# Kernel tuning notes

Hardware: AMD Instinct MI355X
Metric: run time of the kernel (lower is better)

Reference implementation:

```python
import jax, jax.numpy as jnp
import numpy as np

D_MODEL = 2048
N_HEADS = 16
D_HEAD = 128
ROPE_THETA = 10000.0


def _rope(x, offset):
    # x: [B, H, S, D]; half-rotation RoPE with position offset
    B, H, S, D = x.shape
    inv_freq = 1.0 / (ROPE_THETA ** (jnp.arange(0, D, 2, dtype=jnp.float32) / D))  # [D/2]
    pos = (offset + jnp.arange(S, dtype=jnp.float32))                              # [S]
    ang = pos[:, None] * inv_freq[None, :]                                         # [S, D/2]
    cos = jnp.cos(ang).astype(x.dtype)
    sin = jnp.sin(ang).astype(x.dtype)
    x1, x2 = x[..., : D // 2], x[..., D // 2 :]
    return jnp.concatenate([x1 * cos - x2 * sin, x2 * cos + x1 * sin], axis=-1)


def setup_inputs() -> dict:
    key = jax.random.key(0)
    ks = jax.random.split(key, 5)
    B, Sq, Skv = 4, 1024, 1024
    x = jax.random.normal(ks[0], (B, Sq, D_MODEL), dtype=jnp.float32)
    cache_k = jax.random.normal(ks[1], (B, N_HEADS, Skv, D_HEAD), dtype=jnp.float32)
    cache_v = jax.random.normal(ks[2], (B, N_HEADS, Skv, D_HEAD), dtype=jnp.float32)
    w_qkv = jax.random.normal(ks[3], (D_MODEL, 3 * D_MODEL), dtype=jnp.float32) * (D_MODEL ** -0.5)
    w_o = jax.random.normal(ks[4], (D_MODEL, D_MODEL), dtype=jnp.float32) * (D_MODEL ** -0.5)
    return {"x": x, "cache_k": cache_k, "cache_v": cache_v, "w_qkv": w_qkv, "w_o": w_o}


def reference(x, cache_k, cache_v, w_qkv, w_o):
    B, S, _ = x.shape
    offset = cache_k.shape[2]
    # fused QKV projection: [B, S, 3*d_model] -> [B, H, S, 3*d_head]
    qkv = jnp.einsum("bsd,de->bse", x, w_qkv)
    qkv = qkv.reshape(B, S, N_HEADS, 3 * D_HEAD).transpose(0, 2, 1, 3)
    q, k, v = jnp.split(qkv, 3, axis=-1)
    q = _rope(q, offset)
    k = _rope(k, offset)
    # KV-cache concat along sequence dim
    k = jnp.concatenate([cache_k, k], axis=2)  # [B, H, Skv+S, D]
    v = jnp.concatenate([cache_v, v], axis=2)
    # SDPA (no mask, matching mask=None path)
    scale = D_HEAD ** -0.5
    scores = jnp.einsum("bhqd,bhkd->bhqk", q, k) * scale
    attn = jax.nn.softmax(scores, axis=-1)
    out = jnp.einsum("bhqk,bhkd->bhqd", attn, v)           # [B, H, S, D]
    out = out.transpose(0, 2, 1, 3).reshape(B, S, D_MODEL)
    return jnp.einsum("bsd,de->bse", out, w_o)
```

## Files before the change

### kernel.cpp

```cpp
#include <hip/hip_runtime.h>


typedef __bf16 bf16x8 __attribute__((ext_vector_type(8)));
typedef float f32x4 __attribute__((ext_vector_type(4)));
typedef unsigned short u16x8 __attribute__((ext_vector_type(8)));
typedef unsigned short u16x4 __attribute__((ext_vector_type(4)));

__device__ __forceinline__ float b2f(unsigned short u) {
  return __builtin_bit_cast(float, (unsigned int)u << 16);
}
__device__ __forceinline__ unsigned short f2b(float f) {
  unsigned int x = __builtin_bit_cast(unsigned int, f);
  x += 0x7fffu + ((x >> 16) & 1u);
  return (unsigned short)(x >> 16);
}
__device__ __forceinline__ unsigned int cvt_pk_bf16(float lo, float hi) {
  unsigned int r;
  asm("v_cvt_pk_bf16_f32 %0, %1, %2" : "=v"(r) : "v"(lo), "v"(hi));
  return r;
}
__device__ __forceinline__ void gload_lds16(const void* g, void* l) {
  __builtin_amdgcn_global_load_lds(
      (__attribute__((address_space(1))) void*)(g),
      (__attribute__((address_space(3))) void*)(l), 16, 0, 0);
}
__device__ __forceinline__ void barrier_nodrain() {
  asm volatile("" ::: "memory");
  __builtin_amdgcn_s_barrier();
  asm volatile("" ::: "memory");
}

__global__ __launch_bounds__(256) void prep_fused(
    const float* __restrict__ x, const float* __restrict__ ck,
    const float* __restrict__ cv, const float* __restrict__ wqkv,
    const float* __restrict__ wo, unsigned short* __restrict__ xb,
    unsigned short* __restrict__ Kf, unsigned short* __restrict__ Vt,
    unsigned short* __restrict__ wqT, unsigned short* __restrict__ woT,
    float* __restrict__ cs, float* __restrict__ sn) {
  __shared__ float tile[32][33];
  int id = blockIdx.x;
  if (id < 4096) {
    size_t i = ((size_t)id * 256 + threadIdx.x) * 8;
    float4 a = *(const float4*)(x + i);
    float4 b = *(const float4*)(x + i + 4);
    u16x8 v;
    v[0] = f2b(a.x); v[1] = f2b(a.y); v[2] = f2b(a.z); v[3] = f2b(a.w);
    v[4] = f2b(b.x); v[5] = f2b(b.y); v[6] = f2b(b.z); v[7] = f2b(b.w);
    *(u16x8*)(xb + i) = v;
  } else if (id < 20480) {
    const float* in;  unsigned short* out;  int R, C, idx;
    if (id < 16384) { in = wqkv; out = wqT; R = 2048; C = 6144; idx = id - 4096; }
    else            { in = wo;   out = woT; R = 2048; C = 2048; idx = id - 16384; }
    int nc = C >> 5;
    int c0 = (idx % nc) * 32, r0 = (idx / nc) * 32;
    int tx = threadIdx.x & 31, ty = threadIdx.x >> 5;
#pragma unroll
    for (int j = 0; j < 4; ++j)
      tile[ty + j * 8][tx] = in[(size_t)(r0 + ty + j * 8) * C + c0 + tx];
    __syncthreads();
#pragma unroll
    for (int j = 0; j < 4; ++j)
      out[(size_t)(c0 + ty + j * 8) * R + r0 + tx] = f2b(tile[tx][ty + j * 8]);
  } else if (id < 28672) {
    size_t idx = ((size_t)(id - 20480) * 256 + threadIdx.x) * 4;
    size_t bh = idx >> 17, rem = idx & 131071;
    float4 a = *(const float4*)(ck + idx);
    u16x4 v;
    v[0] = f2b(a.x); v[1] = f2b(a.y); v[2] = f2b(a.z); v[3] = f2b(a.w);
    *(u16x4*)(Kf + bh * 262144 + rem) = v;
  } else if (id < 28928) {
    int idx = (id - 28672) * 256 + threadIdx.x;
    int s = idx >> 6, i = idx & 63;
    float inv = exp2f(-(float)i * (13.287712379549449f / 64.0f));
    float ang = (float)(1024 + s) * inv;
    cs[idx] = cosf(ang);
    sn[idx] = sinf(ang);
  } else {
    int idx = id - 28928;
    int bhid = idx >> 7;
    int rem = idx & 127;
    int d0 = (rem >> 5) * 32, s0 = (rem & 31) * 32;
    int tx = threadIdx.x & 31, ty = threadIdx.x >> 5;
#pragma unroll
    for (int j = 0; j < 4; ++j)
      tile[ty + j * 8][tx] = cv[((size_t)bhid * 1024 + s0 + ty + j * 8) * 128 + d0 + tx];
    __syncthreads();
#pragma unroll
    for (int j = 0; j < 4; ++j)
      Vt[((size_t)bhid * 128 + d0 + ty + j * 8) * 2048 + s0 + tx] =
          f2b(tile[tx][ty + j * 8]);
  }
}

template <int M, int N, int K, int MODE>
__global__ __launch_bounds__(512, 4) void gemm_ring(
    const unsigned short* __restrict__ A, const unsigned short* __restrict__ B,
    void* __restrict__ Cout, const float* __restrict__ cs,
    const float* __restrict__ sn, unsigned short* __restrict__ Qb,
    unsigned short* __restrict__ Kf, unsigned short* __restrict__ Vt) {
  __shared__ __align__(16) char lds[3 * 24576];
  constexpr int NT = N / 128;
  constexpr int Kt = K / 32;
  int bid = blockIdx.x;
  int tm = bid / NT, tn = bid % NT;
  int tid = threadIdx.x;
  int lane = tid & 63, wave = tid >> 6;
  int wr = (wave >> 1) * 64;
  int wc1 = wave & 1;
  int l15 = lane & 15, g = lane >> 4;
  int rcol = (g * 16) ^ (((l15 >> 1) & 3) << 4);

  int p = tid * 16;
  int srcCol = (p & 63) ^ (((p >> 7) & 3) << 4);
  const unsigned short* aSrc0 = A + (size_t)(tm * 256 + (p >> 6)) * K + (srcCol >> 1);
  const unsigned short* aSrc1 = aSrc0 + (size_t)128 * K;
  const unsigned short* bSrc  = B + (size_t)(tn * 128 + (p >> 6)) * K + (srcCol >> 1);

  f32x4 acc[4][4] = {};

  auto stage = [&](int s) {
    char* base = (char*)lds + s * 24576;
    gload_lds16(aSrc0, base + p);
    gload_lds16(aSrc1, base + 8192 + p);
    gload_lds16(bSrc,  base + 16384 + p);
    aSrc0 += 32; aSrc1 += 32; bSrc += 32;
  };

  stage(0);
  stage(1);
  asm volatile("s_waitcnt vmcnt(3)" ::: "memory");

  int slot = 0, sNext = 2;
  for (int t = 0; t < Kt; ++t) {
    barrier_nodrain();
    if (t + 2 < Kt) {
      stage(sNext);
      sNext = (sNext == 2) ? 0 : sNext + 1;
      asm volatile("s_waitcnt vmcnt(3)" ::: "memory");
    } else {
      asm volatile("s_waitcnt vmcnt(0)" ::: "memory");
    }
    const char* As_ = (const char*)lds + slot * 24576;
    const char* Bs_ = As_ + 16384;
    bf16x8 af[4], bfr[4];
#pragma unroll
    for (int m = 0; m < 4; ++m)
      af[m] = *(const bf16x8*)(As_ + (wr + m * 16 + l15) * 64 + rcol);
#pragma unroll
    for (int n = 0; n < 4; ++n)
      bfr[n] = *(const bf16x8*)(Bs_ + (wc1 * 16 + n * 32 + l15) * 64 + rcol);
    __builtin_amdgcn_s_setprio(1);
#pragma unroll
    for (int m = 0; m < 4; ++m)
#pragma unroll
      for (int n = 0; n < 4; ++n)
        acc[m][n] = __builtin_amdgcn_mfma_f32_16x16x32_bf16(af[m], bfr[n], acc[m][n], 0, 0, 0);
    __builtin_amdgcn_s_setprio(0);
    slot = (slot == 2) ? 0 : slot + 1;
  }

  if constexpr (MODE == 0) {
#pragma unroll
    for (int m = 0; m < 4; ++m) {
      int row0 = tm * 256 + wr + m * 16 + g * 4;
#pragma unroll
      for (int n = 0; n < 4; ++n) {
        int col = tn * 128 + wc1 * 16 + n * 32 + l15;
#pragma unroll
        for (int r = 0; r < 4; ++r)
          ((float*)Cout)[(size_t)(row0 + r) * N + col] = acc[m][n][r];
      }
    }
  } else {
    int part = tn % 3, h = tn / 3;
    size_t bh = (size_t)(tm >> 2) * 16 + h;
    if (part == 2) {
#pragma unroll
      for (int m = 0; m < 4; ++m) {
        int s0 = (tm & 3) * 256 + wr + m * 16 + g * 4;
#pragma unroll
        for (int n = 0; n < 4; ++n) {
          int d = wc1 * 16 + n * 32 + l15;
          uint2 w;
          w.x = cvt_pk_bf16(acc[m][n][0], acc[m][n][1]);
          w.y = cvt_pk_bf16(acc[m][n][2], acc[m][n][3]);
          *(uint2*)(Vt + (bh * 128 + d) * 2048 + 1024 + s0) = w;
        }
      }
    } else {
      const float qscale = 0.12751738f;
#pragma unroll
      for (int m = 0; m < 4; ++m) {
        int s0 = (tm & 3) * 256 + wr + m * 16 + g * 4;
#pragma unroll
        for (int n = 0; n < 2; ++n) {
          int i1 = wc1 * 16 + n * 32 + l15;
#pragma unroll
          for (int r = 0; r < 4; ++r) {
            int s = s0 + r;
            float c = cs[s * 64 + i1], sv = sn[s * 64 + i1];
            float v1 = acc[m][n][r], v2 = acc[m][n + 2][r];
            float o1 = v1 * c - v2 * sv;
            float o2 = v2 * c + v1 * sv;
            unsigned short* dst;
            if (part == 0) {
              o1 *= qscale; o2 *= qscale;
              dst = Qb + (bh * 1024 + s) * 128;
            } else {
              dst = Kf + (bh * 2048 + 1024 + s) * 128;
            }
            dst[i1] = f2b(o1);
            dst[i1 + 64] = f2b(o2);
          }
        }
      }
    }
  }
}

__global__ __launch_bounds__(256, 2) void attn_kernel(
    const unsigned short* __restrict__ Qb,
    const unsigned short* __restrict__ Kf,
    const unsigned short* __restrict__ Vt,
    unsigned short* __restrict__ Out) {
  __shared__ __align__(16) unsigned short Ks[2][64 * 128];
  __shared__ __align__(16) unsigned short Vs[2][64 * 128];
  __shared__ __align__(16) char PsRaw[4 * 2 * 2048];

  int raw = blockIdx.x;
  int sb = (raw & 7) * 64 + (raw >> 3);
  int bh = sb >> 3, qt = sb & 7;
  int tid = threadIdx.x, lane = tid & 63, wave = tid >> 6;
  int l15 = lane & 15, g = lane >> 4;
  int swz = (l15 & 7) << 4;

  int qrow0 = qt * 128 + wave * 32;
  bf16x8 qf0[4], qf1[4];
  const unsigned short* qp0 = Qb + ((size_t)(bh * 1024 + qrow0 + l15)) * 128;
#pragma unroll
  for (int kk = 0; kk < 4; ++kk) {
    qf0[kk] = *(const bf16x8*)(qp0 + kk * 32 + g * 8);
    qf1[kk] = *(const bf16x8*)(qp0 + 16 * 128 + kk * 32 + g * 8);
  }

  u16x8 ou;
#pragma unroll
  for (int j = 0; j < 8; ++j) ou[j] = 0x3F80;
  bf16x8 ones = __builtin_bit_cast(bf16x8, ou);

  const unsigned short* Kbase = Kf + (size_t)bh * 2048 * 128;
  const unsigned short* Vbase = Vt + (size_t)bh * 128 * 2048;
  const unsigned short* kptr[4];
  const unsigned short* vptr[4];
  char* kdst0[4];
  char* vdst0[4];
#pragma unroll
  for (int is = 0; is < 4; ++is) {
    int p = tid * 16 + is * 4096;
    int lgk = p ^ (((p >> 8) & 7) << 4);
    kptr[is] = Kbase + (size_t)(lgk >> 8) * 128 + ((lgk & 255) >> 1);
    kdst0[is] = (char*)Ks + is * 4096 + (tid & 192) * 16;
    int lgv = p ^ (((p >> 7) & 7) << 4);
    vptr[is] = Vbase + (size_t)(lgv >> 7) * 2048 + ((lgv & 127) >> 1);
    vdst0[is] = (char*)Vs + is * 4096 + (tid & 192) * 16;
  }
  char* ps0 = PsRaw + wave * 4096 + l15 * 128;
  char* ps1 = ps0 + 2048;

  auto stage = [&](int buf) {
#pragma unroll
    for (int is = 0; is < 4; ++is) {
      gload_lds16(kptr[is], kdst0[is] + buf * 16384);  kptr[is] += 64 * 128;
      gload_lds16(vptr[is], vdst0[is] + buf * 16384);  vptr[is] += 64;
    }
  };

  float mrun0 = -1e30f, mrun1 = -1e30f;
  f32x4 acc0[8] = {}, acc1[8] = {};
  f32x4 accl0 = {}, accl1 = {};

  auto softmax_pack = [&](f32x4* st, float& mrun, f32x4* accp, f32x4& accl,
                          char* ps) {
    float m0 = fmaxf(fmaxf(st[0][0], st[0][1]), st[0][2]);
    float m1 = fmaxf(fmaxf(st[0][3], st[1][0]), st[1][1]);
    float m2 = fmaxf(fmaxf(st[1][2], st[1][3]), st[2][0]);
    float m3 = fmaxf(fmaxf(st[2][1], st[2][2]), st[2][3]);
    float m4 = fmaxf(fmaxf(st[3][0], st[3][1]), st[3][2]);
    float pmax = fmaxf(fmaxf(fmaxf(m0, m1), fmaxf(m2, m3)), fmaxf(m4, st[3][3]));
    pmax = fmaxf(pmax, __shfl_xor(pmax, 16));
    pmax = fmaxf(pmax, __shfl_xor(pmax, 32));
    if (!__all(pmax - mrun <= 8.0f)) {
      float mnew = fmaxf(mrun, pmax);
      float corr = exp2f(mrun - mnew);
      accl *= corr;
#pragma unroll
      for (int mt = 0; mt < 8; ++mt) accp[mt] *= corr;
      mrun = mnew;
    }
#pragma unroll
    for (int t = 0; t < 4; ++t) {
      float p0 = exp2f(st[t][0] - mrun);
      float p1 = exp2f(st[t][1] - mrun);
      float p2 = exp2f(st[t][2] - mrun);
      float p3 = exp2f(st[t][3] - mrun);
      uint2 w;
      w.x = cvt_pk_bf16(p0, p1);
      w.y = cvt_pk_bf16(p2, p3);
      *(uint2*)(ps + ((t * 32 + g * 8) ^ swz)) = w;
    }
  };

  stage(0);
  for (int it = 0; it < 32; ++it) {
    int cur = it & 1;
    barrier_nodrain();
    if (it + 1 < 32) {
      stage(cur ^ 1);
      asm volatile("s_waitcnt vmcnt(8)" ::: "memory");
    } else {
      asm volatile("s_waitcnt vmcnt(0)" ::: "memory");
    }
    barrier_nodrain();
    const char* ksA = (const char*)Ks + cur * 16384 + l15 * 256;
    const char* vsA = (const char*)Vs + cur * 16384 + l15 * 128;

    f32x4 st0[4] = {}, st1[4] = {};
#pragma unroll
    for (int kk = 0; kk < 4; ++kk) {
#pragma unroll
      for (int t = 0; t < 4; ++t) {
        bf16x8 a = *(const bf16x8*)(ksA + t * 4096 + ((kk * 64 + g * 16) ^ swz));
        st0[t] = __builtin_amdgcn_mfma_f32_16x16x32_bf16(a, qf0[kk], st0[t], 0, 0, 0);
        st1[t] = __builtin_amdgcn_mfma_f32_16x16x32_bf16(a, qf1[kk], st1[t], 0, 0, 0);
      }
    }

    softmax_pack(st0, mrun0, acc0, accl0, ps0);
    softmax_pack(st1, mrun1, acc1, accl1, ps1);

#pragma unroll
    for (int k2 = 0; k2 < 2; ++k2) {
      bf16x8 p0 = *(const bf16x8*)(ps0 + ((k2 * 64 + g * 16) ^ swz));
      bf16x8 p1 = *(const bf16x8*)(ps1 + ((k2 * 64 + g * 16) ^ swz));
      accl0 = __builtin_amdgcn_mfma_f32_16x16x32_bf16(ones, p0, accl0, 0, 0, 0);
      accl1 = __builtin_amdgcn_mfma_f32_16x16x32_bf16(ones, p1, accl1, 0, 0, 0);
#pragma unroll
      for (int mt = 0; mt < 8; ++mt) {
        bf16x8 a = *(const bf16x8*)(vsA + mt * 2048 + ((k2 * 64 + g * 16) ^ swz));
        acc0[mt] = __builtin_amdgcn_mfma_f32_16x16x32_bf16(a, p0, acc0[mt], 0, 0, 0);
        acc1[mt] = __builtin_amdgcn_mfma_f32_16x16x32_bf16(a, p1, acc1[mt], 0, 0, 0);
      }
    }
  }

  float inv0 = 1.f / accl0[0];
  float inv1 = 1.f / accl1[0];
  int b = bh >> 4, h = bh & 15;
  int sq = qt * 128 + wave * 32 + l15;
  unsigned short* orow0 = Out + ((size_t)(b * 1024 + sq) * 16 + h) * 128;
  unsigned short* orow1 = orow0 + (size_t)16 * 2048;
#pragma unroll
  for (int mt = 0; mt < 8; ++mt) {
    uint2 w0, w1;
    w0.x = cvt_pk_bf16(acc0[mt][0] * inv0, acc0[mt][1] * inv0);
    w0.y = cvt_pk_bf16(acc0[mt][2] * inv0, acc0[mt][3] * inv0);
    w1.x = cvt_pk_bf16(acc1[mt][0] * inv1, acc1[mt][1] * inv1);
    w1.y = cvt_pk_bf16(acc1[mt][2] * inv1, acc1[mt][3] * inv1);
    *(uint2*)(orow0 + mt * 16 + g * 4) = w0;
    *(uint2*)(orow1 + mt * 16 + g * 4) = w1;
  }
}

extern "C" void kernel_launch(void* const* d_in, const int* in_sizes, int n_in,
                              void* d_out, int out_size, void* d_ws, size_t ws_size,
                              hipStream_t stream) {
  const float* x       = (const float*)d_in[0];
  const float* cache_k = (const float*)d_in[1];
  const float* cache_v = (const float*)d_in[2];
  const float* w_qkv   = (const float*)d_in[3];
  const float* w_o     = (const float*)d_in[4];
  float* out = (float*)d_out;

  char* W = (char*)d_ws;
  constexpr size_t O_TRIG = 0;
  constexpr size_t O_XB   = 524288;
  constexpr size_t O_WQT  = O_XB  + 16777216;
  constexpr size_t O_WOT  = O_WQT + 25165824;
  constexpr size_t O_QB   = O_WOT + 8388608;
  constexpr size_t O_KF   = O_QB  + 16777216;
  constexpr size_t O_VT   = O_KF  + 33554432;
  float* cs_tab = (float*)(W + O_TRIG);
  float* sn_tab = (float*)(W + O_TRIG + 262144);
  unsigned short* xb   = (unsigned short*)(W + O_XB);
  unsigned short* wqT  = (unsigned short*)(W + O_WQT);
  unsigned short* woT  = (unsigned short*)(W + O_WOT);
  unsigned short* qb   = (unsigned short*)(W + O_QB);
  unsigned short* Kf   = (unsigned short*)(W + O_KF);
  unsigned short* Vt   = (unsigned short*)(W + O_VT);
  unsigned short* attn_out = xb;

  prep_fused<<<37120, 256, 0, stream>>>(x, cache_k, cache_v, w_qkv, w_o,
                                        xb, Kf, Vt, wqT, woT, cs_tab, sn_tab);
  gemm_ring<4096, 6144, 2048, 1><<<768, 512, 0, stream>>>(
      xb, wqT, nullptr, cs_tab, sn_tab, qb, Kf, Vt);
  attn_kernel<<<512, 256, 0, stream>>>(qb, Kf, Vt, attn_out);
  gemm_ring<4096, 2048, 2048, 0><<<256, 512, 0, stream>>>(
      attn_out, woT, out, nullptr, nullptr, nullptr, nullptr, nullptr);
}
```

Measured before the change: 296.1 us.

## Move cache and W_o conversion into QKV GEMM launch as extra blocks

Splits the prep kernel so only x, W_qkv and the trig tables are converted before the QKV GEMM. The K-cache and V-cache bf16 conversion and the W_o transpose run as extra workgroups appended to the QKV GEMM grid, so this bandwidth-bound work can overlap with the compute-bound GEMM tail. It also remaps block IDs in the GEMM with an 8-way interleave, which changes tile order and possibly cache locality. The extra blocks share the GEMM's large LDS and 512-thread configuration, which may limit occupancy while they run.

After: 297.4 us. No clear change (+0.4%).

```diff
diff --git a/kernel.cpp b/kernel.cpp
--- a/kernel.cpp
+++ b/kernel.cpp
@@ -30,12 +30,9 @@
   asm volatile("" ::: "memory");
 }
 
-__global__ __launch_bounds__(256) void prep_fused(
-    const float* __restrict__ x, const float* __restrict__ ck,
-    const float* __restrict__ cv, const float* __restrict__ wqkv,
-    const float* __restrict__ wo, unsigned short* __restrict__ xb,
-    unsigned short* __restrict__ Kf, unsigned short* __restrict__ Vt,
-    unsigned short* __restrict__ wqT, unsigned short* __restrict__ woT,
+__global__ __launch_bounds__(256) void prep1(
+    const float* __restrict__ x, const float* __restrict__ wqkv,
+    unsigned short* __restrict__ xb, unsigned short* __restrict__ wqT,
     float* __restrict__ cs, float* __restrict__ sn) {
   __shared__ float tile[32][33];
   int id = blockIdx.x;
@@ -47,48 +44,24 @@
     v[0] = f2b(a.x); v[1] = f2b(a.y); v[2] = f2b(a.z); v[3] = f2b(a.w);
     v[4] = f2b(b.x); v[5] = f2b(b.y); v[6] = f2b(b.z); v[7] = f2b(b.w);
     *(u16x8*)(xb + i) = v;
-  } else if (id < 20480) {
-    const float* in;  unsigned short* out;  int R, C, idx;
-    if (id < 16384) { in = wqkv; out = wqT; R = 2048; C = 6144; idx = id - 4096; }
-    else            { in = wo;   out = woT; R = 2048; C = 2048; idx = id - 16384; }
-    int nc = C >> 5;
-    int c0 = (idx % nc) * 32, r0 = (idx / nc) * 32;
+  } else if (id < 16384) {
+    int idx = id - 4096;
+    int c0 = (idx % 192) * 32, r0 = (idx / 192) * 32;
     int tx = threadIdx.x & 31, ty = threadIdx.x >> 5;
 #pragma unroll
     for (int j = 0; j < 4; ++j)
-      tile[ty + j * 8][tx] = in[(size_t)(r0 + ty + j * 8) * C + c0 + tx];
+      tile[ty + j * 8][tx] = wqkv[(size_t)(r0 + ty + j * 8) * 6144 + c0 + tx];
     __syncthreads();
 #pragma unroll
     for (int j = 0; j < 4; ++j)
-      out[(size_t)(c0 + ty + j * 8) * R + r0 + tx] = f2b(tile[tx][ty + j * 8]);
-  } else if (id < 28672) {
-    size_t idx = ((size_t)(id - 20480) * 256 + threadIdx.x) * 4;
-    size_t bh = idx >> 17, rem = idx & 131071;
-    float4 a = *(const float4*)(ck + idx);
-    u16x4 v;
-    v[0] = f2b(a.x); v[1] = f2b(a.y); v[2] = f2b(a.z); v[3] = f2b(a.w);
-    *(u16x4*)(Kf + bh * 262144 + rem) = v;
-  } else if (id < 28928) {
-    int idx = (id - 28672) * 256 + threadIdx.x;
+      wqT[(size_t)(c0 + ty + j * 8) * 2048 + r0 + tx] = f2b(tile[tx][ty + j * 8]);
+  } else {
+    int idx = (id - 16384) * 256 + threadIdx.x;
     int s = idx >> 6, i = idx & 63;
     float inv = exp2f(-(float)i * (13.287712379549449f / 64.0f));
     float ang = (float)(1024 + s) * inv;
     cs[idx] = cosf(ang);
     sn[idx] = sinf(ang);
-  } else {
-    int idx = id - 28928;
-    int bhid = idx >> 7;
-    int rem = idx & 127;
-    int d0 = (rem >> 5) * 32, s0 = (rem & 31) * 32;
-    int tx = threadIdx.x & 31, ty = threadIdx.x >> 5;
-#pragma unroll
-    for (int j = 0; j < 4; ++j)
-      tile[ty + j * 8][tx] = cv[((size_t)bhid * 1024 + s0 + ty + j * 8) * 128 + d0 + tx];
-    __syncthreads();
-#pragma unroll
-    for (int j = 0; j < 4; ++j)
-      Vt[((size_t)bhid * 128 + d0 + ty + j * 8) * 2048 + s0 + tx] =
-          f2b(tile[tx][ty + j * 8]);
   }
 }
 
@@ -97,13 +70,62 @@
     const unsigned short* __restrict__ A, const unsigned short* __restrict__ B,
     void* __restrict__ Cout, const float* __restrict__ cs,
     const float* __restrict__ sn, unsigned short* __restrict__ Qb,
-    unsigned short* __restrict__ Kf, unsigned short* __restrict__ Vt) {
+    unsigned short* __restrict__ Kf, unsigned short* __restrict__ Vt,
+    const float* __restrict__ ck, const float* __restrict__ cv,
+    const float* __restrict__ wo, unsigned short* __restrict__ woT) {
   __shared__ __align__(16) char lds[3 * 24576];
   constexpr int NT = N / 128;
-  constexpr int Kt = K / 32;
-  int bid = blockIdx.x;
+  constexpr int NWG = (M / 256) * NT;
+  int tid = threadIdx.x;
+
+  if constexpr (MODE == 1) {
+    if (blockIdx.x >= NWG) {
+      int aid = blockIdx.x - NWG;
+      if (aid < 4096) {
+        size_t idx = ((size_t)aid * 512 + tid) * 4;
+        size_t bh = idx >> 17, rem = idx & 131071;
+        float4 a = *(const float4*)(ck + idx);
+        u16x4 v;
+        v[0] = f2b(a.x); v[1] = f2b(a.y); v[2] = f2b(a.z); v[3] = f2b(a.w);
+        *(u16x4*)(Kf + bh * 262144 + rem) = v;
+      } else if (aid < 8192) {
+        int t2 = (aid - 4096) * 2 + (tid >> 8);
+        int tl = tid & 255;
+        int bhid = t2 >> 7, rem = t2 & 127;
+        int d0 = (rem >> 5) * 32, s0 = (rem & 31) * 32;
+        int tx = tl & 31, ty = tl >> 5;
+        float(*tile)[33] = (float(*)[33])(lds + (tid >> 8) * 4352);
+#pragma unroll
+        for (int j = 0; j < 4; ++j)
+          tile[ty + j * 8][tx] =
+              cv[((size_t)bhid * 1024 + s0 + ty + j * 8) * 128 + d0 + tx];
+        __syncthreads();
+#pragma unroll
+        for (int j = 0; j < 4; ++j)
+          Vt[((size_t)bhid * 128 + d0 + ty + j * 8) * 2048 + s0 + tx] =
+              f2b(tile[tx][ty + j * 8]);
+      } else {
+        int t2 = (aid - 8192) * 2 + (tid >> 8);
+        int tl = tid & 255;
+        int c0 = (t2 & 63) * 32, r0 = (t2 >> 6) * 32;
+        int tx = tl & 31, ty = tl >> 5;
+        float(*tile)[33] = (float(*)[33])(lds + (tid >> 8) * 4352);
+#pragma unroll
+        for (int j = 0; j < 4; ++j)
+          tile[ty + j * 8][tx] = wo[(size_t)(r0 + ty + j * 8) * 2048 + c0 + tx];
+        __syncthreads();
+#pragma unroll
+        for (int j = 0; j < 4; ++j)
+          woT[(size_t)(c0 + ty + j * 8) * 2048 + r0 + tx] =
+              f2b(tile[tx][ty + j * 8]);
+      }
+      return;
+    }
+  }
+
+  int raw = blockIdx.x;
+  int bid = (raw & 7) * (NWG / 8) + (raw >> 3);
   int tm = bid / NT, tn = bid % NT;
-  int tid = threadIdx.x;
   int lane = tid & 63, wave = tid >> 6;
   int wr = (wave >> 1) * 64;
   int wc1 = wave & 1;
@@ -130,6 +152,7 @@
   stage(1);
   asm volatile("s_waitcnt vmcnt(3)" ::: "memory");
 
+  constexpr int Kt = K / 32;
   int slot = 0, sNext = 2;
   for (int t = 0; t < Kt; ++t) {
     barrier_nodrain();
@@ -399,11 +422,12 @@
   unsigned short* Vt   = (unsigned short*)(W + O_VT);
   unsigned short* attn_out = xb;
 
-  prep_fused<<<37120, 256, 0, stream>>>(x, cache_k, cache_v, w_qkv, w_o,
-                                        xb, Kf, Vt, wqT, woT, cs_tab, sn_tab);
-  gemm_ring<4096, 6144, 2048, 1><<<768, 512, 0, stream>>>(
-      xb, wqT, nullptr, cs_tab, sn_tab, qb, Kf, Vt);
+  prep1<<<16640, 256, 0, stream>>>(x, w_qkv, xb, wqT, cs_tab, sn_tab);
+  gemm_ring<4096, 6144, 2048, 1><<<768 + 10240, 512, 0, stream>>>(
+      xb, wqT, nullptr, cs_tab, sn_tab, qb, Kf, Vt,
+      cache_k, cache_v, w_o, woT);
   attn_kernel<<<512, 256, 0, stream>>>(qb, Kf, Vt, attn_out);
   gemm_ring<4096, 2048, 2048, 0><<<256, 512, 0, stream>>>(
-      attn_out, woT, out, nullptr, nullptr, nullptr, nullptr, nullptr);
-}
+      attn_out, woT, out, nullptr, nullptr, nullptr, nullptr, nullptr,
+      nullptr, nullptr, nullptr, nullptr);
+}
```
